# Performance work log

Hardware: AMD Instinct MI355X
Metric: run time of the kernel (lower is better)

## Reference

```python
import jax, jax.numpy as jnp
import numpy as np

V = 32000   # vocab_size
D = 1024    # dim
H = 16      # n_heads
HD = D // H # head_dim = 64
R = 64      # kv_lora_rank (must equal HD for this module's matmul to be valid)
E = 32      # n_routed_experts
K = 8       # n_activated_experts
F = 1024    # moe_inter_dim
I = 4096    # inter_dim (shared experts)
NS = 2      # n_shared_experts
B, S = 2, 1024
EPS = 1e-5
THETA = 10000.0


def setup_inputs() -> dict:
    key = jax.random.key(0)
    ks = iter(jax.random.split(key, 32))
    def nrm(shape, scale=0.02):
        return jax.random.normal(next(ks), shape, jnp.float32) * scale
    return {
        "input_ids": jax.random.randint(next(ks), (B, S), 0, V),
        "emb": nrm((V, D)),
        "Wq": nrm((D, D)), "Wk": nrm((D, R)), "Wv": nrm((D, R)), "Wo": nrm((D, D)),
        "g1": jnp.ones((D,), jnp.float32), "beta1": jnp.zeros((D,), jnp.float32),
        "g2": jnp.ones((D,), jnp.float32), "beta2": jnp.zeros((D,), jnp.float32),
        "Wr": nrm((D, E)), "br": jnp.zeros((E,), jnp.float32),
        "We1": nrm((E, D, F)), "be1": jnp.zeros((E, F), jnp.float32),
        "We2": nrm((E, F, D)), "be2": jnp.zeros((E, D), jnp.float32),
        "Ws1": nrm((NS, D, I)), "bs1": jnp.zeros((NS, I), jnp.float32),
        "Ws2": nrm((NS, I, D)), "bs2": jnp.zeros((NS, D), jnp.float32),
        "Wout": nrm((D, V)), "bout": jnp.zeros((V,), jnp.float32),
    }


def _layernorm(x, g, b):
    mu = x.mean(-1, keepdims=True)
    var = jnp.mean((x - mu) ** 2, -1, keepdims=True)
    return (x - mu) * jax.lax.rsqrt(var + EPS) * g + b


def _rope(x):
    # x: [B, S, H, hd]; interleaved even/odd rotation, per the torch RotaryEmbedding
    hd, s = x.shape[-1], x.shape[1]
    freqs = 1.0 / (THETA ** (jnp.arange(0, hd, 2, dtype=jnp.float32) / hd))
    ang = jnp.arange(s, dtype=jnp.float32)[:, None] * freqs        # [S, hd/2]
    cos = jnp.cos(ang)[None, :, None, :]
    sin = jnp.sin(ang)[None, :, None, :]
    xe, xo = x[..., ::2], x[..., 1::2]
    xr = cos * xe - sin * xo
    yr = cos * xo + sin * xe
    return jnp.stack([xr, yr], -1).reshape(x.shape)


def _forward(input_ids, emb, Wq, Wk, Wv, Wo, g1, beta1, g2, beta2,
             Wr, br, We1, be1, We2, be2, Ws1, bs1, Ws2, bs2, Wout, bout):
    b, s = input_ids.shape
    x = emb[input_ids]                                             # [B,S,D]

    # --- attention sublayer ---
    h = _layernorm(x, g1, beta1)
    q = (h @ Wq).reshape(b, s, H, HD)
    k = (h @ Wk).reshape(b, s, 1, R)
    v = (h @ Wv).reshape(b, s, 1, R)
    q = _rope(q)
    k = _rope(k)
    scores = jnp.einsum('bshd,bskd->bshk', q, k) / np.float32(np.sqrt(HD))  # [B,S,H,1]
    attn = jax.nn.softmax(scores, axis=-1)                         # size-1 axis -> ones (faithful)
    out = jnp.einsum('bshk,bskd->bshd', attn, v).reshape(b, s, D)
    x = x + out @ Wo

    # --- MoE sublayer ---
    h = _layernorm(x, g2, beta2)
    t = h.reshape(-1, D)                                           # [T,D]
    T = t.shape[0]
    probs = jax.nn.softmax(t @ Wr + br, axis=-1)                   # [T,E]
    w, idx = jax.lax.top_k(probs, K)                               # [T,K]
    w = w / w.sum(-1, keepdims=True)
    # combine[t,e] = sum of normalized weights of slots routed to expert e
    combine = jnp.zeros((T, E), t.dtype).at[jnp.arange(T)[:, None], idx].add(w)

    def body(acc, p):
        W1, b1, W2, b2, c = p
        y = jax.nn.silu(t @ W1 + b1) @ W2 + b2                     # [T,D]
        return acc + c[:, None] * y, None

    moe_out, _ = jax.lax.scan(body, jnp.zeros_like(t), (We1, be1, We2, be2, combine.T))

    shared = jnp.zeros_like(t)
    for sidx in range(NS):
        shared = shared + jax.nn.silu(t @ Ws1[sidx] + bs1[sidx]) @ Ws2[sidx] + bs2[sidx]

    x = x + (moe_out + shared).reshape(b, s, D)

    return x @ Wout + bout                                         # [B,S,V]


def reference(input_ids, emb, Wq, Wk, Wv, Wo, g1, beta1, g2, beta2,
              Wr, br, We1, be1, We2, be2, Ws1, bs1, Ws2, bs2, Wout, bout):
    return _forward(input_ids, emb, Wq, Wk, Wv, Wo, g1, beta1, g2, beta2,
                    Wr, br, We1, be1, We2, be2, Ws1, bs1, Ws2, bs2, Wout, bout)
```

## Files before the change

kernel.cpp:

```cpp
#include <hip/hip_runtime.h>
#include <hip/hip_bf16.h>

#define DEV __device__ __forceinline__

typedef __attribute__((ext_vector_type(8))) __bf16 bf16x8;
typedef __attribute__((ext_vector_type(4))) float f32x4;

DEV unsigned short f2bf(float f) {
  unsigned u = __builtin_bit_cast(unsigned, f);
  u = (u + 0x7fffu + ((u >> 16) & 1u)) >> 16;
  return (unsigned short)u;
}
DEV float bf2f(unsigned short h) {
  unsigned u = ((unsigned)h) << 16;
  return __builtin_bit_cast(float, u);
}

DEV void gload16(const void* g, void* l) {
  __builtin_amdgcn_global_load_lds((__attribute__((address_space(1))) void*)(g),
                                   (__attribute__((address_space(3))) void*)(l),
                                   16, 0, 0);
}

__global__ __launch_bounds__(256) void k_transpose(const float* __restrict__ src,
                                                   unsigned short* __restrict__ dst,
                                                   int R, int C, long sB, long dB) {
  src += (long)blockIdx.z * sB;
  dst += (long)blockIdx.z * dB;
  __shared__ float tile[32][33];
  int tx = threadIdx.x & 31, ty = threadIdx.x >> 5;
  int c0 = blockIdx.x * 32, r0 = blockIdx.y * 32;
#pragma unroll
  for (int rr = ty; rr < 32; rr += 8) tile[rr][tx] = src[(long)(r0 + rr) * C + c0 + tx];
  __syncthreads();
#pragma unroll
  for (int cc = ty; cc < 32; cc += 8)
    dst[(long)(c0 + cc) * R + r0 + tx] = f2bf(tile[tx][cc]);
}

__global__ __launch_bounds__(256) void k_embed_ln(const int* __restrict__ ids,
                                                  const float* __restrict__ emb,
                                                  const float* __restrict__ g,
                                                  const float* __restrict__ b,
                                                  float* __restrict__ x, float* __restrict__ h) {
  int t = blockIdx.x, tid = threadIdx.x;
  long base = (long)ids[t] * 1024;
  float4 v = ((const float4*)(emb + base))[tid];
  float s = v.x + v.y + v.z + v.w;
  float ss = v.x * v.x + v.y * v.y + v.z * v.z + v.w * v.w;
  for (int o = 32; o; o >>= 1) { s += __shfl_xor(s, o); ss += __shfl_xor(ss, o); }
  __shared__ float rs[4], rss[4];
  int wv = tid >> 6;
  if ((tid & 63) == 0) { rs[wv] = s; rss[wv] = ss; }
  __syncthreads();
  s = rs[0] + rs[1] + rs[2] + rs[3];
  ss = rss[0] + rss[1] + rss[2] + rss[3];
  float mu = s * (1.f / 1024.f);
  float rstd = rsqrtf(ss * (1.f / 1024.f) - mu * mu + 1e-5f);
  float4 gg = ((const float4*)g)[tid];
  float4 bb = ((const float4*)b)[tid];
  float4 o4;
  o4.x = (v.x - mu) * rstd * gg.x + bb.x;
  o4.y = (v.y - mu) * rstd * gg.y + bb.y;
  o4.z = (v.z - mu) * rstd * gg.z + bb.z;
  o4.w = (v.w - mu) * rstd * gg.w + bb.w;
  ((float4*)(x + (long)t * 1024))[tid] = v;
  ((float4*)(h + (long)t * 1024))[tid] = o4;
}

__global__ __launch_bounds__(64) void k_vgemm(const float* __restrict__ h,
                                              const float* __restrict__ Wv,
                                              float* __restrict__ v) {
  int j = threadIdx.x;
  int b = blockIdx.x * 16;
  float acc[16];
#pragma unroll
  for (int tt = 0; tt < 16; tt++) acc[tt] = 0.f;
  for (int k = 0; k < 1024; k++) {
    float wv = Wv[k * 64 + j];
#pragma unroll
    for (int tt = 0; tt < 16; tt++) acc[tt] += h[(long)(b + tt) * 1024 + k] * wv;
  }
#pragma unroll
  for (int tt = 0; tt < 16; tt++) v[(long)(b + tt) * 64 + j] = acc[tt];
}

__global__ __launch_bounds__(256) void k_woeff(const float* __restrict__ Wo,
                                               float* __restrict__ woeff) {
  int i = blockIdx.x * 256 + threadIdx.x;
  int d = i >> 10, c = i & 1023;
  float s = 0.f;
#pragma unroll
  for (int hh = 0; hh < 16; hh++) s += Wo[(long)(hh * 64 + d) * 1024 + c];
  woeff[i] = s;
}

__global__ __launch_bounds__(256) void k_attn_ln2(const float* __restrict__ x,
                                                  const float* __restrict__ v,
                                                  const float* __restrict__ woeff,
                                                  const float* __restrict__ g,
                                                  const float* __restrict__ b,
                                                  float* __restrict__ x2,
                                                  float* __restrict__ t32,
                                                  unsigned short* __restrict__ tbf) {
  int t = blockIdx.x, tid = threadIdx.x;
  __shared__ float vr[64];
  __shared__ float rs[4], rss[4];
  if (tid < 64) vr[tid] = v[t * 64 + tid];
  __syncthreads();
  float4 a = ((const float4*)(x + (long)t * 1024))[tid];
  float4 acc = {0.f, 0.f, 0.f, 0.f};
#pragma unroll 16
  for (int d = 0; d < 64; d++) {
    float4 w = ((const float4*)(woeff + d * 1024))[tid];
    float vd = vr[d];
    acc.x += vd * w.x; acc.y += vd * w.y; acc.z += vd * w.z; acc.w += vd * w.w;
  }
  a.x += acc.x; a.y += acc.y; a.z += acc.z; a.w += acc.w;
  ((float4*)(x2 + (long)t * 1024))[tid] = a;
  float s = a.x + a.y + a.z + a.w;
  float ss = a.x * a.x + a.y * a.y + a.z * a.z + a.w * a.w;
  for (int o = 32; o; o >>= 1) { s += __shfl_xor(s, o); ss += __shfl_xor(ss, o); }
  int wv = tid >> 6;
  if ((tid & 63) == 0) { rs[wv] = s; rss[wv] = ss; }
  __syncthreads();
  s = rs[0] + rs[1] + rs[2] + rs[3];
  ss = rss[0] + rss[1] + rss[2] + rss[3];
  float mu = s * (1.f / 1024.f);
  float rstd = rsqrtf(ss * (1.f / 1024.f) - mu * mu + 1e-5f);
  float4 gg = ((const float4*)g)[tid];
  float4 bb = ((const float4*)b)[tid];
  float4 o4;
  o4.x = (a.x - mu) * rstd * gg.x + bb.x;
  o4.y = (a.y - mu) * rstd * gg.y + bb.y;
  o4.z = (a.z - mu) * rstd * gg.z + bb.z;
  o4.w = (a.w - mu) * rstd * gg.w + bb.w;
  ((float4*)(t32 + (long)t * 1024))[tid] = o4;
  ushort4 ob;
  ob.x = f2bf(o4.x); ob.y = f2bf(o4.y); ob.z = f2bf(o4.z); ob.w = f2bf(o4.w);
  ((ushort4*)(tbf + (long)t * 1024))[tid] = ob;
}

__global__ __launch_bounds__(64) void k_router(const float* __restrict__ t32,
                                               const float* __restrict__ Wr,
                                               const float* __restrict__ br,
                                               int* __restrict__ ridx, float* __restrict__ rw) {
  int t = blockIdx.x, lane = threadIdx.x;
  float acc = -1e30f;
  if (lane < 32) {
    float s = 0.f;
    const float* tr = t32 + (long)t * 1024;
#pragma unroll 8
    for (int k = 0; k < 1024; k++) s += tr[k] * Wr[k * 32 + lane];
    acc = s + br[lane];
  }
  float cur = acc, top0 = 0.f, denom = 0.f, my_e = 0.f;
  int my_i = 0;
#pragma unroll
  for (int r = 0; r < 8; r++) {
    float v = cur;
    int bi = lane;
    for (int o = 32; o; o >>= 1) {
      float ov = __shfl_xor(v, o);
      int oi = __shfl_xor(bi, o);
      if (ov > v || (ov == v && oi < bi)) { v = ov; bi = oi; }
    }
    if (r == 0) top0 = v;
    float e = __expf(v - top0);
    denom += e;
    if (lane == r) { my_i = bi; my_e = e; }
    if (lane == bi) cur = -1e30f;
  }
  if (lane < 8) {
    ridx[t * 8 + lane] = my_i;
    rw[t * 8 + lane] = my_e / denom;
  }
}

__global__ __launch_bounds__(256) void k_build(const int* __restrict__ ridx,
                                               const float* __restrict__ rw,
                                               int* __restrict__ tok_of,
                                               int* __restrict__ slot_of,
                                               int* __restrict__ tile_e) {
  __shared__ int cnt[32], base_slot[32], cur[32];
  int tid = threadIdx.x;
  if (tid < 32) { cnt[tid] = 0; cur[tid] = 0; }
  __syncthreads();
  for (int i = tid; i < 16384; i += 256) atomicAdd(&cnt[ridx[i]], 1);
  __syncthreads();
  if (tid == 0) {
    int tile = 0;
    for (int e = 0; e < 32; e++) {
      base_slot[e] = tile * 128;
      int nt = (cnt[e] + 127) >> 7;
      for (int j = 0; j < nt; j++) tile_e[tile++] = e;
    }
    for (; tile < 160; tile++) tile_e[tile] = -1;
  }
  __syncthreads();
  for (int s = tid; s < 20480; s += 256) tok_of[s] = 0;
  __syncthreads();
  for (int i = tid; i < 16384; i += 256) {
    int e = ridx[i];
    int pos = atomicAdd(&cur[e], 1);
    int slot = base_slot[e] + pos;
    tok_of[slot] = i >> 3;
    slot_of[i] = slot;
  }
  (void)rw;
}

template <int SILU, int OBF16, int MOE>
__global__ __launch_bounds__(256) void k_gemm(const unsigned short* __restrict__ A, long aStride,
                                              int lda, const unsigned short* __restrict__ BT,
                                              long bStride, const float* __restrict__ bias,
                                              int biasStride, void* __restrict__ Cv, long cStride,
                                              int ldc, int K, const int* __restrict__ rowmap,
                                              const int* __restrict__ tile_e) {
  __shared__ unsigned short As[4096];
  __shared__ unsigned short Bs[4096];
  int tid = threadIdx.x, lane = tid & 63, wave = tid >> 6;
  int n0 = blockIdx.x * 128;
  int row0 = blockIdx.y * 128;
  unsigned short* Cb = (unsigned short*)Cv;
  float* Cf = (float*)Cv;
  if (MOE) {
    int e = tile_e[blockIdx.y];
    if (e < 0) return;
    BT += (long)e * bStride;
    bias += (long)e * biasStride;
  } else {
    int z = blockIdx.z;
    A += (long)z * aStride;
    BT += (long)z * bStride;
    bias += (long)z * biasStride;
    Cb += (long)z * cStride;
    Cf += (long)z * cStride;
  }
  const unsigned short* gA[2];
  const unsigned short* gB[2];
  char* dA[2];
  char* dB[2];
  int colb = (lane & 3) * 8;
#pragma unroll
  for (int i = 0; i < 2; i++) {
    int rl = i * 64 + wave * 16 + (lane >> 2);
    int ar;
    if (MOE) ar = rowmap ? rowmap[row0 + rl] : (row0 + rl);
    else ar = row0 + rl;
    gA[i] = A + (long)ar * lda + colb;
    gB[i] = BT + (long)(n0 + rl) * K + colb;
    dA[i] = (char*)As + i * 4096 + wave * 1024;
    dB[i] = (char*)Bs + i * 4096 + wave * 1024;
  }
  int l16 = lane & 15, quad = lane >> 4;
  int wm = wave >> 1, wn = wave & 1;
  const unsigned short* pa = As + (wm * 64 + l16) * 32 + quad * 8;
  const unsigned short* pb = Bs + (wn * 64 + l16) * 32 + quad * 8;
  f32x4 acc[4][4] = {};
  for (int kt = 0; kt < K; kt += 32) {
    __syncthreads();
    gload16(gA[0] + kt, dA[0]);
    gload16(gA[1] + kt, dA[1]);
    gload16(gB[0] + kt, dB[0]);
    gload16(gB[1] + kt, dB[1]);
    __syncthreads();
    bf16x8 av[4], bv[4];
#pragma unroll
    for (int i = 0; i < 4; i++) {
      av[i] = *(const bf16x8*)(pa + i * 512);
      bv[i] = *(const bf16x8*)(pb + i * 512);
    }
#pragma unroll
    for (int i = 0; i < 4; i++)
#pragma unroll
      for (int j = 0; j < 4; j++)
        acc[i][j] = __builtin_amdgcn_mfma_f32_16x16x32_bf16(av[i], bv[j], acc[i][j], 0, 0, 0);
  }
#pragma unroll
  for (int j = 0; j < 4; j++) {
    int col = n0 + wn * 64 + j * 16 + l16;
    float bb = bias[col];
#pragma unroll
    for (int i = 0; i < 4; i++) {
#pragma unroll
      for (int r = 0; r < 4; r++) {
        int row = row0 + wm * 64 + i * 16 + quad * 4 + r;
        float v = acc[i][j][r] + bb;
        if (SILU) v = v / (1.f + __expf(-v));
        if (OBF16) Cb[(long)row * ldc + col] = f2bf(v);
        else Cf[(long)row * ldc + col] = v;
      }
    }
  }
}

__global__ __launch_bounds__(256) void k_fuse(const float* __restrict__ x2,
                                              const float* __restrict__ csh,
                                              const unsigned short* __restrict__ Y,
                                              const int* __restrict__ slot_of,
                                              const float* __restrict__ rw,
                                              unsigned short* __restrict__ xfbf) {
  int t = blockIdx.x, tid = threadIdx.x;
  __shared__ int sl[8];
  __shared__ float sw[8];
  if (tid < 8) {
    sl[tid] = slot_of[t * 8 + tid];
    sw[tid] = rw[t * 8 + tid];
  }
  __syncthreads();
  float4 a = ((const float4*)(x2 + (long)t * 1024))[tid];
  float4 c0 = ((const float4*)(csh + (long)t * 1024))[tid];
  float4 c1 = ((const float4*)(csh + (long)(2048 + t) * 1024))[tid];
  float ax = a.x + c0.x + c1.x, ay = a.y + c0.y + c1.y;
  float az = a.z + c0.z + c1.z, aw = a.w + c0.w + c1.w;
#pragma unroll
  for (int r = 0; r < 8; r++) {
    ushort4 y = ((const ushort4*)(Y + (long)sl[r] * 1024))[tid];
    float w = sw[r];
    ax += w * bf2f(y.x); ay += w * bf2f(y.y);
    az += w * bf2f(y.z); aw += w * bf2f(y.w);
  }
  ushort4 o;
  o.x = f2bf(ax); o.y = f2bf(ay); o.z = f2bf(az); o.w = f2bf(aw);
  ((ushort4*)(xfbf + (long)t * 1024))[tid] = o;
}

extern "C" void kernel_launch(void* const* d_in, const int* in_sizes, int n_in, void* d_out,
                              int out_size, void* d_ws, size_t ws_size, hipStream_t stream) {
  const int* ids = (const int*)d_in[0];
  const float* emb = (const float*)d_in[1];
  const float* Wv = (const float*)d_in[4];
  const float* Wo = (const float*)d_in[5];
  const float* g1 = (const float*)d_in[6];
  const float* beta1 = (const float*)d_in[7];
  const float* g2 = (const float*)d_in[8];
  const float* beta2 = (const float*)d_in[9];
  const float* Wr = (const float*)d_in[10];
  const float* br = (const float*)d_in[11];
  const float* We1 = (const float*)d_in[12];
  const float* be1 = (const float*)d_in[13];
  const float* We2 = (const float*)d_in[14];
  const float* be2 = (const float*)d_in[15];
  const float* Ws1 = (const float*)d_in[16];
  const float* bs1 = (const float*)d_in[17];
  const float* Ws2 = (const float*)d_in[18];
  const float* bs2 = (const float*)d_in[19];
  const float* Wout = (const float*)d_in[20];
  const float* bout = (const float*)d_in[21];
  (void)in_sizes; (void)n_in; (void)out_size; (void)ws_size;

  char* w = (char*)d_ws;
  auto alloc = [&](size_t n) {
    char* p = w;
    w += (n + 255) & ~(size_t)255;
    return p;
  };
  unsigned short* We1T = (unsigned short*)alloc(32ull * 1024 * 1024 * 2);
  unsigned short* We2T = (unsigned short*)alloc(32ull * 1024 * 1024 * 2);
  unsigned short* Ws1T = (unsigned short*)alloc(2ull * 4096 * 1024 * 2);
  unsigned short* Ws2T = (unsigned short*)alloc(2ull * 4096 * 1024 * 2);
  unsigned short* WoutT = (unsigned short*)alloc(32000ull * 1024 * 2);
  float* x = (float*)alloc(2048ull * 1024 * 4);
  float* h = (float*)alloc(2048ull * 1024 * 4);
  float* v = (float*)alloc(2048ull * 64 * 4);
  float* woeff = (float*)alloc(64ull * 1024 * 4);
  float* x2 = (float*)alloc(2048ull * 1024 * 4);
  float* t32 = (float*)alloc(2048ull * 1024 * 4);
  unsigned short* tbf = (unsigned short*)alloc(2048ull * 1024 * 2);
  int* ridx = (int*)alloc(16384ull * 4);
  float* rw = (float*)alloc(16384ull * 4);
  int* tok_of = (int*)alloc(20480ull * 4);
  int* slot_of = (int*)alloc(16384ull * 4);
  int* tile_e = (int*)alloc(256ull * 4);
  unsigned short* Ush = (unsigned short*)alloc(2ull * 2048 * 4096 * 2);
  float* Csh = (float*)alloc(2ull * 2048 * 1024 * 4);
  unsigned short* Umoe = (unsigned short*)alloc(20480ull * 1024 * 2);
  unsigned short* Y = (unsigned short*)alloc(20480ull * 1024 * 2);
  unsigned short* xfbf = (unsigned short*)alloc(2048ull * 1024 * 2);

  dim3 B256(256);
  k_transpose<<<dim3(32, 32, 32), B256, 0, stream>>>(We1, We1T, 1024, 1024, 1024L * 1024, 1024L * 1024);
  k_transpose<<<dim3(32, 32, 32), B256, 0, stream>>>(We2, We2T, 1024, 1024, 1024L * 1024, 1024L * 1024);
  k_transpose<<<dim3(128, 32, 2), B256, 0, stream>>>(Ws1, Ws1T, 1024, 4096, 4096L * 1024, 4096L * 1024);
  k_transpose<<<dim3(32, 128, 2), B256, 0, stream>>>(Ws2, Ws2T, 4096, 1024, 4096L * 1024, 4096L * 1024);
  k_transpose<<<dim3(1000, 32, 1), B256, 0, stream>>>(Wout, WoutT, 1024, 32000, 0, 0);

  k_embed_ln<<<2048, B256, 0, stream>>>(ids, emb, g1, beta1, x, h);
  k_vgemm<<<128, 64, 0, stream>>>(h, Wv, v);
  k_woeff<<<256, B256, 0, stream>>>(Wo, woeff);
  k_attn_ln2<<<2048, B256, 0, stream>>>(x, v, woeff, g2, beta2, x2, t32, tbf);
  k_router<<<2048, 64, 0, stream>>>(t32, Wr, br, ridx, rw);
  k_build<<<1, B256, 0, stream>>>(ridx, rw, tok_of, slot_of, tile_e);

  k_gemm<1, 1, 0><<<dim3(32, 16, 2), B256, 0, stream>>>(tbf, 0L, 1024, Ws1T, 4096L * 1024, bs1,
                                                        4096, Ush, 2048L * 4096, 4096, 1024,
                                                        nullptr, nullptr);
  k_gemm<0, 0, 0><<<dim3(8, 16, 2), B256, 0, stream>>>(Ush, 2048L * 4096, 4096, Ws2T, 1024L * 4096,
                                                       bs2, 1024, Csh, 2048L * 1024, 1024, 4096,
                                                       nullptr, nullptr);
  k_gemm<1, 1, 1><<<dim3(8, 160, 1), B256, 0, stream>>>(tbf, 0L, 1024, We1T, 1024L * 1024, be1,
                                                        1024, Umoe, 0L, 1024, 1024, tok_of, tile_e);
  k_gemm<0, 1, 1><<<dim3(8, 160, 1), B256, 0, stream>>>(Umoe, 0L, 1024, We2T, 1024L * 1024, be2,
                                                        1024, Y, 0L, 1024, 1024, nullptr, tile_e);
  k_fuse<<<2048, B256, 0, stream>>>(x2, Csh, Y, slot_of, rw, xfbf);
  k_gemm<0, 0, 0><<<dim3(250, 16, 1), B256, 0, stream>>>(xfbf, 0L, 1024, WoutT, 0L, bout, 0,
                                                         (float*)d_out, 0L, 32000, 1024, nullptr,
                                                         nullptr);
}
```

Baseline: 1.599 ms.

## Vectorize transpose, vgemm and router; swap output GEMM grid order with nontemporal stores

The weight transposes now use 64x64 tiles with float4 loads and ushort4 stores. The V projection stages four token rows in shared memory, one wave per token. The router runs four tokens per block, splits the K dimension across half-waves and loads activations as float4. The final vocab GEMM swaps its grid order so consecutive blocks share the same B tile, and writes its large fp32 output with nontemporal stores. Together these aim to cut memory-bound overhead in the preprocessing kernels and the output write, at the cost of more shared memory per block and different cache behaviour.

```diff
diff --git a/kernel.cpp b/kernel.cpp
--- a/kernel.cpp
+++ b/kernel.cpp
@@ -27,15 +27,27 @@
                                                    int R, int C, long sB, long dB) {
   src += (long)blockIdx.z * sB;
   dst += (long)blockIdx.z * dB;
-  __shared__ float tile[32][33];
-  int tx = threadIdx.x & 31, ty = threadIdx.x >> 5;
-  int c0 = blockIdx.x * 32, r0 = blockIdx.y * 32;
-#pragma unroll
-  for (int rr = ty; rr < 32; rr += 8) tile[rr][tx] = src[(long)(r0 + rr) * C + c0 + tx];
-  __syncthreads();
-#pragma unroll
-  for (int cc = ty; cc < 32; cc += 8)
-    dst[(long)(c0 + cc) * R + r0 + tx] = f2bf(tile[tx][cc]);
+  __shared__ float tile[64][65];
+  int tx = threadIdx.x & 15, ty = threadIdx.x >> 4;
+  int c0 = blockIdx.x * 64, r0 = blockIdx.y * 64;
+#pragma unroll
+  for (int rr = ty; rr < 64; rr += 16) {
+    float4 v = *(const float4*)(src + (long)(r0 + rr) * C + c0 + tx * 4);
+    tile[rr][tx * 4 + 0] = v.x;
+    tile[rr][tx * 4 + 1] = v.y;
+    tile[rr][tx * 4 + 2] = v.z;
+    tile[rr][tx * 4 + 3] = v.w;
+  }
+  __syncthreads();
+#pragma unroll
+  for (int cc = ty; cc < 64; cc += 16) {
+    ushort4 o;
+    o.x = f2bf(tile[tx * 4 + 0][cc]);
+    o.y = f2bf(tile[tx * 4 + 1][cc]);
+    o.z = f2bf(tile[tx * 4 + 2][cc]);
+    o.w = f2bf(tile[tx * 4 + 3][cc]);
+    *(ushort4*)(dst + (long)(c0 + cc) * R + r0 + tx * 4) = o;
+  }
 }
 
 __global__ __launch_bounds__(256) void k_embed_ln(const int* __restrict__ ids,
@@ -68,21 +80,28 @@
   ((float4*)(h + (long)t * 1024))[tid] = o4;
 }
 
-__global__ __launch_bounds__(64) void k_vgemm(const float* __restrict__ h,
-                                              const float* __restrict__ Wv,
-                                              float* __restrict__ v) {
-  int j = threadIdx.x;
-  int b = blockIdx.x * 16;
-  float acc[16];
-#pragma unroll
-  for (int tt = 0; tt < 16; tt++) acc[tt] = 0.f;
-  for (int k = 0; k < 1024; k++) {
-    float wv = Wv[k * 64 + j];
-#pragma unroll
-    for (int tt = 0; tt < 16; tt++) acc[tt] += h[(long)(b + tt) * 1024 + k] * wv;
-  }
-#pragma unroll
-  for (int tt = 0; tt < 16; tt++) v[(long)(b + tt) * 64 + j] = acc[tt];
+__global__ __launch_bounds__(256) void k_vgemm(const float* __restrict__ h,
+                                               const float* __restrict__ Wv,
+                                               float* __restrict__ v) {
+  __shared__ float hs[4][1024];
+  int tid = threadIdx.x;
+  int t0 = blockIdx.x * 4;
+#pragma unroll
+  for (int i = 0; i < 4; i++) {
+    int idx = tid + i * 256;
+    ((float4*)hs)[idx] = ((const float4*)(h + (long)t0 * 1024))[idx];
+  }
+  __syncthreads();
+  int wave = tid >> 6, lane = tid & 63;
+  const float* hr = hs[wave];
+  float acc = 0.f;
+#pragma unroll 4
+  for (int k = 0; k < 1024; k += 4) {
+    float4 hv = *(const float4*)(hr + k);
+    acc += hv.x * Wv[(k + 0) * 64 + lane] + hv.y * Wv[(k + 1) * 64 + lane] +
+           hv.z * Wv[(k + 2) * 64 + lane] + hv.w * Wv[(k + 3) * 64 + lane];
+  }
+  v[(long)(t0 + wave) * 64 + lane] = acc;
 }
 
 __global__ __launch_bounds__(256) void k_woeff(const float* __restrict__ Wo,
@@ -141,25 +160,30 @@
   ((ushort4*)(tbf + (long)t * 1024))[tid] = ob;
 }
 
-__global__ __launch_bounds__(64) void k_router(const float* __restrict__ t32,
-                                               const float* __restrict__ Wr,
-                                               const float* __restrict__ br,
-                                               int* __restrict__ ridx, float* __restrict__ rw) {
-  int t = blockIdx.x, lane = threadIdx.x;
-  float acc = -1e30f;
-  if (lane < 32) {
-    float s = 0.f;
-    const float* tr = t32 + (long)t * 1024;
-#pragma unroll 8
-    for (int k = 0; k < 1024; k++) s += tr[k] * Wr[k * 32 + lane];
-    acc = s + br[lane];
-  }
+__global__ __launch_bounds__(256) void k_router(const float* __restrict__ t32,
+                                                const float* __restrict__ Wr,
+                                                const float* __restrict__ br,
+                                                int* __restrict__ ridx, float* __restrict__ rw) {
+  int wave = threadIdx.x >> 6, lane = threadIdx.x & 63;
+  int t = blockIdx.x * 4 + wave;
+  int n = lane & 31, half = lane >> 5;
+  const float* tr = t32 + (long)t * 1024 + half * 512;
+  const float* wr = Wr + (long)half * 512 * 32 + n;
+  float s = 0.f;
+#pragma unroll 4
+  for (int k = 0; k < 512; k += 4) {
+    float4 tv = *(const float4*)(tr + k);
+    s += tv.x * wr[(k + 0) * 32] + tv.y * wr[(k + 1) * 32] + tv.z * wr[(k + 2) * 32] +
+         tv.w * wr[(k + 3) * 32];
+  }
+  s += __shfl_xor(s, 32);
+  float acc = (half == 0) ? s + br[n] : -1e30f;
   float cur = acc, top0 = 0.f, denom = 0.f, my_e = 0.f;
   int my_i = 0;
 #pragma unroll
   for (int r = 0; r < 8; r++) {
     float v = cur;
-    int bi = lane;
+    int bi = n;
     for (int o = 32; o; o >>= 1) {
       float ov = __shfl_xor(v, o);
       int oi = __shfl_xor(bi, o);
@@ -169,7 +193,7 @@
     float e = __expf(v - top0);
     denom += e;
     if (lane == r) { my_i = bi; my_e = e; }
-    if (lane == bi) cur = -1e30f;
+    if (half == 0 && n == bi) cur = -1e30f;
   }
   if (lane < 8) {
     ridx[t * 8 + lane] = my_i;
@@ -210,7 +234,7 @@
   (void)rw;
 }
 
-template <int SILU, int OBF16, int MOE>
+template <int SILU, int OBF16, int MOE, int SWAPXY, int NT>
 __global__ __launch_bounds__(256) void k_gemm(const unsigned short* __restrict__ A, long aStride,
                                               int lda, const unsigned short* __restrict__ BT,
                                               long bStride, const float* __restrict__ bias,
@@ -220,12 +244,14 @@
   __shared__ unsigned short As[4096];
   __shared__ unsigned short Bs[4096];
   int tid = threadIdx.x, lane = tid & 63, wave = tid >> 6;
-  int n0 = blockIdx.x * 128;
-  int row0 = blockIdx.y * 128;
+  int bx = SWAPXY ? blockIdx.y : blockIdx.x;
+  int by = SWAPXY ? blockIdx.x : blockIdx.y;
+  int n0 = bx * 128;
+  int row0 = by * 128;
   unsigned short* Cb = (unsigned short*)Cv;
   float* Cf = (float*)Cv;
   if (MOE) {
-    int e = tile_e[blockIdx.y];
+    int e = tile_e[by];
     if (e < 0) return;
     BT += (long)e * bStride;
     bias += (long)e * biasStride;
@@ -288,8 +314,13 @@
         int row = row0 + wm * 64 + i * 16 + quad * 4 + r;
         float v = acc[i][j][r] + bb;
         if (SILU) v = v / (1.f + __expf(-v));
-        if (OBF16) Cb[(long)row * ldc + col] = f2bf(v);
-        else Cf[(long)row * ldc + col] = v;
+        if (OBF16) {
+          Cb[(long)row * ldc + col] = f2bf(v);
+        } else if (NT) {
+          __builtin_nontemporal_store(v, &Cf[(long)row * ldc + col]);
+        } else {
+          Cf[(long)row * ldc + col] = v;
+        }
       }
     }
   }
@@ -380,31 +411,34 @@
   unsigned short* xfbf = (unsigned short*)alloc(2048ull * 1024 * 2);
 
   dim3 B256(256);
-  k_transpose<<<dim3(32, 32, 32), B256, 0, stream>>>(We1, We1T, 1024, 1024, 1024L * 1024, 1024L * 1024);
-  k_transpose<<<dim3(32, 32, 32), B256, 0, stream>>>(We2, We2T, 1024, 1024, 1024L * 1024, 1024L * 1024);
-  k_transpose<<<dim3(128, 32, 2), B256, 0, stream>>>(Ws1, Ws1T, 1024, 4096, 4096L * 1024, 4096L * 1024);
-  k_transpose<<<dim3(32, 128, 2), B256, 0, stream>>>(Ws2, Ws2T, 4096, 1024, 4096L * 1024, 4096L * 1024);
-  k_transpose<<<dim3(1000, 32, 1), B256, 0, stream>>>(Wout, WoutT, 1024, 32000, 0, 0);
+  k_transpose<<<dim3(16, 16, 32), B256, 0, stream>>>(We1, We1T, 1024, 1024, 1024L * 1024, 1024L * 1024);
+  k_transpose<<<dim3(16, 16, 32), B256, 0, stream>>>(We2, We2T, 1024, 1024, 1024L * 1024, 1024L * 1024);
+  k_transpose<<<dim3(64, 16, 2), B256, 0, stream>>>(Ws1, Ws1T, 1024, 4096, 4096L * 1024, 4096L * 1024);
+  k_transpose<<<dim3(16, 64, 2), B256, 0, stream>>>(Ws2, Ws2T, 4096, 1024, 4096L * 1024, 4096L * 1024);
+  k_transpose<<<dim3(500, 16, 1), B256, 0, stream>>>(Wout, WoutT, 1024, 32000, 0, 0);
 
   k_embed_ln<<<2048, B256, 0, stream>>>(ids, emb, g1, beta1, x, h);
-  k_vgemm<<<128, 64, 0, stream>>>(h, Wv, v);
+  k_vgemm<<<512, B256, 0, stream>>>(h, Wv, v);
   k_woeff<<<256, B256, 0, stream>>>(Wo, woeff);
   k_attn_ln2<<<2048, B256, 0, stream>>>(x, v, woeff, g2, beta2, x2, t32, tbf);
-  k_router<<<2048, 64, 0, stream>>>(t32, Wr, br, ridx, rw);
+  k_router<<<512, B256, 0, stream>>>(t32, Wr, br, ridx, rw);
   k_build<<<1, B256, 0, stream>>>(ridx, rw, tok_of, slot_of, tile_e);
 
-  k_gemm<1, 1, 0><<<dim3(32, 16, 2), B256, 0, stream>>>(tbf, 0L, 1024, Ws1T, 4096L * 1024, bs1,
-                                                        4096, Ush, 2048L * 4096, 4096, 1024,
-                                                        nullptr, nullptr);
-  k_gemm<0, 0, 0><<<dim3(8, 16, 2), B256, 0, stream>>>(Ush, 2048L * 4096, 4096, Ws2T, 1024L * 4096,
-                                                       bs2, 1024, Csh, 2048L * 1024, 1024, 4096,
-                                                       nullptr, nullptr);
-  k_gemm<1, 1, 1><<<dim3(8, 160, 1), B256, 0, stream>>>(tbf, 0L, 1024, We1T, 1024L * 1024, be1,
-                                                        1024, Umoe, 0L, 1024, 1024, tok_of, tile_e);
-  k_gemm<0, 1, 1><<<dim3(8, 160, 1), B256, 0, stream>>>(Umoe, 0L, 1024, We2T, 1024L * 1024, be2,
-                                                        1024, Y, 0L, 1024, 1024, nullptr, tile_e);
+  k_gemm<1, 1, 0, 0, 0><<<dim3(32, 16, 2), B256, 0, stream>>>(tbf, 0L, 1024, Ws1T, 4096L * 1024,
+                                                              bs1, 4096, Ush, 2048L * 4096, 4096,
+                                                              1024, nullptr, nullptr);
+  k_gemm<0, 0, 0, 0, 0><<<dim3(8, 16, 2), B256, 0, stream>>>(Ush, 2048L * 4096, 4096, Ws2T,
+                                                             1024L * 4096, bs2, 1024, Csh,
+                                                             2048L * 1024, 1024, 4096, nullptr,
+                                                             nullptr);
+  k_gemm<1, 1, 1, 0, 0><<<dim3(8, 160, 1), B256, 0, stream>>>(tbf, 0L, 1024, We1T, 1024L * 1024,
+                                                              be1, 1024, Umoe, 0L, 1024, 1024,
+                                                              tok_of, tile_e);
+  k_gemm<0, 1, 1, 0, 0><<<dim3(8, 160, 1), B256, 0, stream>>>(Umoe, 0L, 1024, We2T, 1024L * 1024,
+                                                              be2, 1024, Y, 0L, 1024, 1024,
+                                                              nullptr, tile_e);
   k_fuse<<<2048, B256, 0, stream>>>(x2, Csh, Y, slot_of, rw, xfbf);
-  k_gemm<0, 0, 0><<<dim3(250, 16, 1), B256, 0, stream>>>(xfbf, 0L, 1024, WoutT, 0L, bout, 0,
-                                                         (float*)d_out, 0L, 32000, 1024, nullptr,
-                                                         nullptr);
-}
+  k_gemm<0, 0, 0, 1, 1><<<dim3(16, 250, 1), B256, 0, stream>>>(xfbf, 0L, 1024, WoutT, 0L, bout, 0,
+                                                               (float*)d_out, 0L, 32000, 1024,
+                                                               nullptr, nullptr);
+}
```

After: 1.353 ms. -15.4%, faster.
